# Kernel tuning notes

Hardware: AMD Instinct MI355X
Metric: run time of the kernel (lower is better)

## Reference

```python
import jax, jax.numpy as jnp
import numpy as np

B, T, D = 4, 2048, 2048
H = 16
HO = D // H  # head_out = 128


def setup_inputs() -> dict:
    key = jax.random.key(0)
    ks = jax.random.split(key, 6)
    x = jax.random.normal(ks[0], (B, T, D), dtype=jnp.float32)
    scale = 0.02
    Wq = jax.random.normal(ks[1], (D, D), dtype=jnp.float32) * scale
    Wk = jax.random.normal(ks[2], (D, D), dtype=jnp.float32) * scale
    Wv = jax.random.normal(ks[3], (D, D), dtype=jnp.float32) * scale
    Wp = jax.random.normal(ks[4], (D, D), dtype=jnp.float32) * scale
    bp = jnp.zeros((D,), dtype=jnp.float32)
    return {"x": x, "Wq": Wq, "Wk": Wk, "Wv": Wv, "Wp": Wp, "bp": bp}


def reference(x, Wq, Wk, Wv, Wp, bp):
    b, t, _ = x.shape
    # QKV projections (weights stored [d_in, d_out])
    q = x @ Wq
    k = x @ Wk
    v = x @ Wv
    split = lambda a: a.reshape(b, t, H, HO).transpose(0, 2, 1, 3)  # [b,H,T,ho]
    qh, kh, vh = split(q), split(k), split(v)
    # Feature attention: contract over tokens -> [b,H,ho,ho]
    scores = jnp.einsum('bhtf,bhtg->bhfg', qh, kh) / jnp.sqrt(jnp.float32(HO))
    weights = jax.nn.softmax(scores, axis=-1)  # dropout p=0.0 (identity)
    # feature_alibi: [1/T, 1/(T-1), ..., 1], broadcast over batch/head/feature
    feat_alibi = (1.0 / jnp.arange(t, 0, -1, dtype=jnp.float32)).reshape(1, 1, t, 1)
    vh = vh + feat_alibi
    # (weights @ v^T)^T : ctx[b,h,t,f] = sum_g weights[b,h,f,g] * v[b,h,t,g]
    ctx = jnp.einsum('bhfg,bhtg->bhtf', weights, vh)
    ctx = ctx.transpose(0, 2, 1, 3).reshape(b, t, H * HO)  # [b,T,d_out]
    return ctx @ Wp + bp
```

## Files before the change

kernel.cpp:

```cpp
#include <hip/hip_runtime.h>
#include <hip/hip_bf16.h>


#define Tt 2048
#define Dd 2048
#define Mm 8192

typedef __attribute__((ext_vector_type(4))) float f32x4;
typedef __attribute__((ext_vector_type(8))) short s16x8;
static_assert(sizeof(s16x8) == 16, "frag size");

typedef const __attribute__((address_space(1))) void* gptr_t;
typedef __attribute__((address_space(3))) void* lptr_t;

__device__ __forceinline__ float bf2f(ushort u) {
    union { unsigned int i; float f; } c; c.i = ((unsigned int)u) << 16; return c.f;
}
__device__ __forceinline__ ushort f2bf(float f) {
    union { float f; unsigned int i; } c; c.f = f;
    return (ushort)((c.i + 0x7FFFu + ((c.i >> 16) & 1u)) >> 16);
}
__device__ __forceinline__ void gload16(const void* g, void* l) {
    __builtin_amdgcn_global_load_lds((gptr_t)g, (lptr_t)l, 16, 0, 0);
}
__device__ __forceinline__ s16x8 ldfrag(const char* p) { return *(const s16x8*)p; }

#define MFMA_BF16(d, a, b) \
    d = __builtin_amdgcn_mfma_f32_16x16x32_bf16((a), (b), (d), 0, 0, 0)


__global__ __launch_bounds__(256) void convxT_kernel(const float* __restrict__ x,
        ushort* __restrict__ xb, ushort* __restrict__ xT) {
    __shared__ float tile[64][65];
    const int b = blockIdx.z;
    const int t0 = blockIdx.y * 64, d0 = blockIdx.x * 64;
    const int r4 = threadIdx.x >> 6, c = threadIdx.x & 63;
#pragma unroll
    for (int i = 0; i < 16; i++) {
        const int row = i * 4 + r4;
        const size_t g = ((size_t)b * Tt + t0 + row) * Dd + d0 + c;
        const float val = x[g];
        xb[g] = f2bf(val);
        tile[row][c] = val;
    }
    __syncthreads();
#pragma unroll
    for (int i = 0; i < 16; i++) {
        const int row = i * 4 + r4;
        xT[(size_t)b * ((size_t)Dd * Tt) + (size_t)(d0 + row) * Tt + t0 + c] =
            f2bf(tile[c][row]);
    }
}


__global__ __launch_bounds__(256) void transw_kernel(const float* __restrict__ W0,
        const float* __restrict__ W1, const float* __restrict__ W2,
        const float* __restrict__ W3, ushort* __restrict__ Wt,
        float* __restrict__ S) {
    __shared__ float tile[64][65];
    const int z = blockIdx.z;
    const float* W = (z == 0) ? W0 : (z == 1) ? W1 : (z == 2) ? W2 : W3;
    ushort* dst = Wt + (size_t)z * ((size_t)Dd * Dd);
    const int n0 = blockIdx.x * 64, k0 = blockIdx.y * 64;
    const int r4 = threadIdx.x >> 6, c = threadIdx.x & 63;
#pragma unroll
    for (int i = 0; i < 16; i++) {
        const int row = i * 4 + r4;
        tile[row][c] = W[(size_t)(k0 + row) * Dd + n0 + c];
    }
    __syncthreads();
#pragma unroll
    for (int i = 0; i < 16; i++) {
        const int row = i * 4 + r4;
        dst[(size_t)(n0 + row) * Dd + k0 + c] = f2bf(tile[c][row]);
    }
    if (z == 3) {
        float partial = 0.f;
#pragma unroll
        for (int i = 0; i < 16; i++) partial += tile[r4 * 16 + i][c];
        atomicAdd(&S[n0 + c], partial);
    }
}


__device__ __forceinline__ void stage_half(char* ldsRegion, const ushort* gRegion,
                                           int ld, int half, int tid) {
#pragma unroll
    for (int j = 0; j < 2; j++) {
        const int Pb = half * 16384 + j * 8192 + (tid >> 6) * 1024;
        const int P = Pb + (tid & 63) * 16;
        const int row = P >> 7;
        const int colb = (P ^ ((row & 7) << 4)) & 127;
        gload16(gRegion + (size_t)row * ld + (colb >> 1), ldsRegion + Pb);
    }
}

template <int MODE>
__global__ __launch_bounds__(512, 2) void gemm256_kernel(
        const ushort* __restrict__ A, const ushort* __restrict__ Bt,
        void* __restrict__ Cv, const float* __restrict__ bias,
        const float* __restrict__ S,
        int Kdim, int lda, int ldb, int ldc,
        size_t astride, size_t bstride, size_t cstride) {
    extern __shared__ char lds[];

    const int tid = threadIdx.x;
    const int lane = tid & 63;
    const int w = tid >> 6;
    const int wr = w >> 2, wc = w & 3;
    const int fr = lane & 15, fq = lane >> 4;

    const int bid = blockIdx.x;
    const int cpx = (int)gridDim.x >> 3;
    const int wg = (bid & 7) * cpx + (bid >> 3);
    const int m0 = (wg >> 3) * 256;
    const int n0 = (wg & 7) * 256;

    const ushort* Ag = A + (size_t)blockIdx.z * astride + (size_t)m0 * lda;
    const ushort* Bg = Bt + (size_t)blockIdx.z * bstride + (size_t)n0 * ldb;
    const int NT = Kdim >> 6;

    const int aoff = wr * 16384 + fr * 128;
    const int boff = wc * 8192 + fr * 128;
    const int xo = (fr & 7) << 4;
    const int cp0 = (fq * 16) ^ xo;
    const int cp1 = (64 + fq * 16) ^ xo;

    char* buf0 = lds;
    char* buf1 = lds + 65536;
    const char* Ab0 = buf0 + aoff;
    const char* Bb0 = buf0 + 32768 + boff;
    const char* Ab1 = buf1 + aoff;
    const char* Bb1 = buf1 + 32768 + boff;

    f32x4 acc[8][4];
#pragma unroll
    for (int i = 0; i < 8; i++)
#pragma unroll
        for (int j = 0; j < 4; j++) acc[i][j] = {0.f, 0.f, 0.f, 0.f};

    s16x8 afX[4][2], afY[4][2], bf01[2][2], bf23[2][2];

    {
        stage_half(buf0,         Ag, lda, 0, tid);
        stage_half(buf0,         Ag, lda, 1, tid);
        stage_half(buf0 + 32768, Bg, ldb, 0, tid);
        stage_half(buf0 + 32768, Bg, ldb, 1, tid);
        stage_half(buf1,         Ag + 64, lda, 0, tid);
        stage_half(buf1,         Ag + 64, lda, 1, tid);
        stage_half(buf1 + 32768, Bg + 64, ldb, 0, tid);
        stage_half(buf1 + 32768, Bg + 64, ldb, 1, tid);
        __builtin_amdgcn_sched_barrier(0);
        asm volatile("s_waitcnt vmcnt(8)" ::: "memory");
        __builtin_amdgcn_s_barrier();
    }

    const int NI = NT >> 1;
    for (int j = 0; j < NI; ++j) {
        const int e = 2 * j;
        const bool sAo = (j > 0);
        const bool sE2 = (e + 2 < NT);
        const bool sO2 = (e + 3 < NT);
        const ushort* AgO  = Ag + (size_t)(e + 1) * 64;
        const ushort* AgE2 = Ag + (size_t)(e + 2) * 64;
        const ushort* BgE2 = Bg + (size_t)(e + 2) * 64;
        const ushort* BgO2 = Bg + (size_t)(e + 3) * 64;

#pragma unroll
        for (int m = 0; m < 4; m++) {
            afX[m][0] = ldfrag(Ab0 + m * 2048 + cp0);
            afX[m][1] = ldfrag(Ab0 + m * 2048 + cp1);
        }
#pragma unroll
        for (int n = 0; n < 2; n++) {
            bf01[n][0] = ldfrag(Bb0 + n * 2048 + cp0);
            bf01[n][1] = ldfrag(Bb0 + n * 2048 + cp1);
        }
        if (sAo) stage_half(buf1, AgO, lda, 0, tid);
        __builtin_amdgcn_sched_barrier(0);
        asm volatile("s_waitcnt lgkmcnt(8)" ::: "memory");
        __builtin_amdgcn_s_barrier();
        asm volatile("s_waitcnt lgkmcnt(0)" ::: "memory");
        __builtin_amdgcn_sched_barrier(0);
        __builtin_amdgcn_s_setprio(1);
#pragma unroll
        for (int k = 0; k < 2; k++)
#pragma unroll
            for (int m = 0; m < 4; m++)
#pragma unroll
                for (int n = 0; n < 2; n++) MFMA_BF16(acc[m][n], afX[m][k], bf01[n][k]);
        __builtin_amdgcn_s_setprio(0);
        __builtin_amdgcn_s_barrier();

#pragma unroll
        for (int n = 0; n < 2; n++) {
            bf23[n][0] = ldfrag(Bb0 + (n + 2) * 2048 + cp0);
            bf23[n][1] = ldfrag(Bb0 + (n + 2) * 2048 + cp1);
        }
        if (sAo) stage_half(buf1, AgO, lda, 1, tid);
        __builtin_amdgcn_sched_barrier(0);
        __builtin_amdgcn_s_barrier();
        asm volatile("s_waitcnt lgkmcnt(0)" ::: "memory");
        __builtin_amdgcn_sched_barrier(0);
        __builtin_amdgcn_s_setprio(1);
#pragma unroll
        for (int k = 0; k < 2; k++)
#pragma unroll
            for (int m = 0; m < 4; m++)
#pragma unroll
                for (int n = 0; n < 2; n++) MFMA_BF16(acc[m][n + 2], afX[m][k], bf23[n][k]);
        __builtin_amdgcn_s_setprio(0);
        __builtin_amdgcn_s_barrier();

#pragma unroll
        for (int m = 0; m < 4; m++) {
            afY[m][0] = ldfrag(Ab0 + (m + 4) * 2048 + cp0);
            afY[m][1] = ldfrag(Ab0 + (m + 4) * 2048 + cp1);
        }
        if (sE2) stage_half(buf0 + 32768, BgE2, ldb, 0, tid);
        __builtin_amdgcn_sched_barrier(0);
        __builtin_amdgcn_s_barrier();
        asm volatile("s_waitcnt lgkmcnt(0)" ::: "memory");
        __builtin_amdgcn_sched_barrier(0);
        __builtin_amdgcn_s_setprio(1);
#pragma unroll
        for (int k = 0; k < 2; k++)
#pragma unroll
            for (int m = 0; m < 4; m++)
#pragma unroll
                for (int n = 0; n < 2; n++) MFMA_BF16(acc[m + 4][n], afY[m][k], bf01[n][k]);
        __builtin_amdgcn_s_setprio(0);
        __builtin_amdgcn_s_barrier();

        if (sE2) stage_half(buf0 + 32768, BgE2, ldb, 1, tid);
        __builtin_amdgcn_sched_barrier(0);
        __builtin_amdgcn_s_setprio(1);
#pragma unroll
        for (int k = 0; k < 2; k++)
#pragma unroll
            for (int m = 0; m < 4; m++)
#pragma unroll
                for (int n = 0; n < 2; n++) MFMA_BF16(acc[m + 4][n + 2], afY[m][k], bf23[n][k]);
        __builtin_amdgcn_s_setprio(0);
        __builtin_amdgcn_sched_barrier(0);
        if (sE2) asm volatile("s_waitcnt vmcnt(4)" ::: "memory");
        else     asm volatile("s_waitcnt vmcnt(0)" ::: "memory");
        __builtin_amdgcn_s_barrier();

#pragma unroll
        for (int m = 0; m < 4; m++) {
            afX[m][0] = ldfrag(Ab1 + m * 2048 + cp0);
            afX[m][1] = ldfrag(Ab1 + m * 2048 + cp1);
        }
#pragma unroll
        for (int n = 0; n < 2; n++) {
            bf01[n][0] = ldfrag(Bb1 + n * 2048 + cp0);
            bf01[n][1] = ldfrag(Bb1 + n * 2048 + cp1);
        }
        if (sE2) stage_half(buf0, AgE2, lda, 0, tid);
        __builtin_amdgcn_sched_barrier(0);
        asm volatile("s_waitcnt lgkmcnt(8)" ::: "memory");
        __builtin_amdgcn_s_barrier();
        asm volatile("s_waitcnt lgkmcnt(0)" ::: "memory");
        __builtin_amdgcn_sched_barrier(0);
        __builtin_amdgcn_s_setprio(1);
#pragma unroll
        for (int k = 0; k < 2; k++)
#pragma unroll
            for (int m = 0; m < 4; m++)
#pragma unroll
                for (int n = 0; n < 2; n++) MFMA_BF16(acc[m][n], afX[m][k], bf01[n][k]);
        __builtin_amdgcn_s_setprio(0);
        __builtin_amdgcn_s_barrier();

#pragma unroll
        for (int n = 0; n < 2; n++) {
            bf23[n][0] = ldfrag(Bb1 + (n + 2) * 2048 + cp0);
            bf23[n][1] = ldfrag(Bb1 + (n + 2) * 2048 + cp1);
        }
        if (sE2) stage_half(buf0, AgE2, lda, 1, tid);
        __builtin_amdgcn_sched_barrier(0);
        __builtin_amdgcn_s_barrier();
        asm volatile("s_waitcnt lgkmcnt(0)" ::: "memory");
        __builtin_amdgcn_sched_barrier(0);
        __builtin_amdgcn_s_setprio(1);
#pragma unroll
        for (int k = 0; k < 2; k++)
#pragma unroll
            for (int m = 0; m < 4; m++)
#pragma unroll
                for (int n = 0; n < 2; n++) MFMA_BF16(acc[m][n + 2], afX[m][k], bf23[n][k]);
        __builtin_amdgcn_s_setprio(0);
        __builtin_amdgcn_s_barrier();

#pragma unroll
        for (int m = 0; m < 4; m++) {
            afY[m][0] = ldfrag(Ab1 + (m + 4) * 2048 + cp0);
            afY[m][1] = ldfrag(Ab1 + (m + 4) * 2048 + cp1);
        }
        if (sO2) stage_half(buf1 + 32768, BgO2, ldb, 0, tid);
        __builtin_amdgcn_sched_barrier(0);
        __builtin_amdgcn_s_barrier();
        asm volatile("s_waitcnt lgkmcnt(0)" ::: "memory");
        __builtin_amdgcn_sched_barrier(0);
        __builtin_amdgcn_s_setprio(1);
#pragma unroll
        for (int k = 0; k < 2; k++)
#pragma unroll
            for (int m = 0; m < 4; m++)
#pragma unroll
                for (int n = 0; n < 2; n++) MFMA_BF16(acc[m + 4][n], afY[m][k], bf01[n][k]);
        __builtin_amdgcn_s_setprio(0);
        __builtin_amdgcn_s_barrier();

        if (sO2) stage_half(buf1 + 32768, BgO2, ldb, 1, tid);
        __builtin_amdgcn_sched_barrier(0);
        __builtin_amdgcn_s_setprio(1);
#pragma unroll
        for (int k = 0; k < 2; k++)
#pragma unroll
            for (int m = 0; m < 4; m++)
#pragma unroll
                for (int n = 0; n < 2; n++) MFMA_BF16(acc[m + 4][n + 2], afY[m][k], bf23[n][k]);
        __builtin_amdgcn_s_setprio(0);
        __builtin_amdgcn_sched_barrier(0);
        if (sO2) asm volatile("s_waitcnt vmcnt(4)" ::: "memory");
        else     asm volatile("s_waitcnt vmcnt(0)" ::: "memory");
        __builtin_amdgcn_s_barrier();
    }

    if (MODE == 2) {
        float* C = (float*)Cv + (size_t)blockIdx.z * cstride;
#pragma unroll
        for (int mi = 0; mi < 8; mi++)
#pragma unroll
            for (int ni = 0; ni < 4; ni++)
#pragma unroll
                for (int r = 0; r < 4; r++) {
                    const int row = m0 + wr * 128 + mi * 16 + fq * 4 + r;
                    const int col = n0 + wc * 64 + ni * 16 + fr;
                    const float alibi = 1.0f / (float)(Tt - row);
                    C[(size_t)row * ldc + col] =
                        acc[mi][ni][r] + alibi * S[col] + bias[col];
                }
    } else {
        ushort* C = (ushort*)Cv + (size_t)blockIdx.z * cstride;
#pragma unroll
        for (int mi = 0; mi < 8; mi++)
#pragma unroll
            for (int ni = 0; ni < 4; ni++)
#pragma unroll
                for (int r = 0; r < 4; r++) {
                    const int row = m0 + wr * 128 + mi * 16 + fq * 4 + r;
                    const int col = n0 + wc * 64 + ni * 16 + fr;
                    C[(size_t)row * ldc + col] = f2bf(acc[mi][ni][r]);
                }
    }
}


template <int MODE>
__global__ __launch_bounds__(256, 2) void gemm_kernel(
        const ushort* __restrict__ A, const ushort* __restrict__ Bt,
        void* __restrict__ Cv,
        int Kdim, int lda, int ldb, int ldc) {
    __shared__ ushort lsA[128 * 32];
    __shared__ ushort lsB[128 * 32];

    const int tid = threadIdx.x;
    const int w = tid >> 6, lane = tid & 63;
    const int m0 = blockIdx.y * 128;
    const int n0 = blockIdx.x * 128;

    const ushort* Ab = A;
    const ushort* Bb = Bt;
    size_t coff = 0;
    if (MODE == 3) {
        const int z = blockIdx.z, s = z >> 6, bh = z & 63;
        const int b = bh >> 4, h = bh & 15;
        Ab += (size_t)h * 128 * Dd + (size_t)s * 512;
        Bb += (size_t)b * ((size_t)Dd * Dd) + (size_t)h * 128 * Dd + (size_t)s * 512;
        coff = (size_t)s * (64 * 16384) + (size_t)bh * 16384;
    }
    if (MODE == 4) {
        const int z = blockIdx.z, b = z >> 4, h = z & 15;
        Ab += (size_t)h * 128;
        Bb += (size_t)z * 16384;
        coff = (size_t)b * ((size_t)Dd * Dd) + (size_t)h * 128;
    }

    const int sr = lane >> 2;
    const int sc = (lane & 3) * 8;
    const int c0 = w, c1 = w + 4;
    const int rA0 = c0 * 16 + sr, rA1 = c1 * 16 + sr;

    const int fr = lane & 15, fq = lane >> 4;
    const int wr = (w >> 1) * 64, wc = (w & 1) * 64;

    f32x4 acc[4][4];
#pragma unroll
    for (int i = 0; i < 4; i++)
#pragma unroll
        for (int j = 0; j < 4; j++) acc[i][j] = {0.f, 0.f, 0.f, 0.f};

    for (int kt = 0; kt < Kdim; kt += 32) {
        gload16(Ab + (size_t)(m0 + rA0) * lda + kt + sc, lsA + c0 * 512);
        gload16(Ab + (size_t)(m0 + rA1) * lda + kt + sc, lsA + c1 * 512);
        gload16(Bb + (size_t)(n0 + rA0) * ldb + kt + sc, lsB + c0 * 512);
        gload16(Bb + (size_t)(n0 + rA1) * ldb + kt + sc, lsB + c1 * 512);
        __syncthreads();

        s16x8 afrag[4], bfrag[4];
#pragma unroll
        for (int i = 0; i < 4; i++)
            afrag[i] = *(const s16x8*)(lsA + (wr + i * 16 + fr) * 32 + fq * 8);
#pragma unroll
        for (int j = 0; j < 4; j++)
            bfrag[j] = *(const s16x8*)(lsB + (wc + j * 16 + fr) * 32 + fq * 8);
#pragma unroll
        for (int i = 0; i < 4; i++)
#pragma unroll
            for (int j = 0; j < 4; j++)
                MFMA_BF16(acc[i][j], afrag[i], bfrag[j]);
        __syncthreads();
    }

    if (MODE == 3) {
        float* C = (float*)Cv + coff;
#pragma unroll
        for (int i = 0; i < 4; i++)
#pragma unroll
            for (int j = 0; j < 4; j++)
#pragma unroll
                for (int r = 0; r < 4; r++) {
                    const int row = m0 + wr + i * 16 + fq * 4 + r;
                    const int col = n0 + wc + j * 16 + fr;
                    C[(size_t)row * ldc + col] = acc[i][j][r];
                }
    } else {
        ushort* C = (ushort*)Cv + coff;
#pragma unroll
        for (int i = 0; i < 4; i++)
#pragma unroll
            for (int j = 0; j < 4; j++)
#pragma unroll
                for (int r = 0; r < 4; r++) {
                    const int row = m0 + wr + i * 16 + fq * 4 + r;
                    const int col = n0 + wc + j * 16 + fr;
                    C[(size_t)row * ldc + col] = f2bf(acc[i][j][r]);
                }
    }
}


__global__ __launch_bounds__(256) void softmax_kernel(const float* __restrict__ part,
                                                      ushort* __restrict__ wtsT) {
    const int tid = threadIdx.x;
    const int wv = tid >> 6, lane = tid & 63;
    const int row = blockIdx.x * 4 + wv;
    const float* p = part + (size_t)row * 128 + lane * 2;
    float v0 = 0.f, v1 = 0.f;
#pragma unroll
    for (int s = 0; s < 4; s++) {
        const float2 t = *(const float2*)(p + (size_t)s * 1048576);
        v0 += t.x; v1 += t.y;
    }
    const float sc = 0.088388347648318447f;
    v0 *= sc; v1 *= sc;
    float m = fmaxf(v0, v1);
#pragma unroll
    for (int off = 32; off > 0; off >>= 1) m = fmaxf(m, __shfl_xor(m, off));
    const float e0 = __expf(v0 - m), e1 = __expf(v1 - m);
    float smv = e0 + e1;
#pragma unroll
    for (int off = 32; off > 0; off >>= 1) smv += __shfl_xor(smv, off);
    const float inv = 1.0f / smv;
    const int bh = row >> 7, f = row & 127;
    ushort* o = wtsT + (size_t)bh * 16384 + (size_t)(lane * 2) * 128 + f;
    o[0]   = f2bf(e0 * inv);
    o[128] = f2bf(e1 * inv);
}


extern "C" void kernel_launch(void* const* d_in, const int* in_sizes, int n_in,
                              void* d_out, int out_size, void* d_ws, size_t ws_size,
                              hipStream_t stream) {
    const float* x  = (const float*)d_in[0];
    const float* Wq = (const float*)d_in[1];
    const float* Wk = (const float*)d_in[2];
    const float* Wv = (const float*)d_in[3];
    const float* Wp = (const float*)d_in[4];
    const float* bp = (const float*)d_in[5];
    float* out = (float*)d_out;
    char* ws = (char*)d_ws;

    ushort* xb   = (ushort*)(ws);
    ushort* xT   = (ushort*)(ws + (32ull << 20));
    ushort* Wt   = (ushort*)(ws + (64ull << 20));
    ushort* G    = (ushort*)(ws + (96ull << 20));
    ushort* Hb   = (ushort*)(ws + (128ull << 20));
    ushort* v    = (ushort*)(ws + (160ull << 20));
    float*  part = (float*) (ws + (96ull << 20));
    ushort* wtsT = (ushort*)(ws + (112ull << 20));
    float*  S    = (float*) (ws + (194ull << 20));
    ushort* Mt   = xT;

    const size_t WSZ = (size_t)Dd * Dd;
    const size_t TD  = (size_t)Tt * Dd;

    static_cast<void>(hipFuncSetAttribute((const void*)gemm256_kernel<0>,
        hipFuncAttributeMaxDynamicSharedMemorySize, 131072));
    static_cast<void>(hipFuncSetAttribute((const void*)gemm256_kernel<2>,
        hipFuncAttributeMaxDynamicSharedMemorySize, 131072));

    static_cast<void>(hipMemsetAsync(S, 0, Dd * sizeof(float), stream));
    convxT_kernel<<<dim3(32, 32, 4), 256, 0, stream>>>(x, xb, xT);
    transw_kernel<<<dim3(32, 32, 4), 256, 0, stream>>>(Wq, Wk, Wv, Wp, Wt, S);

    gemm256_kernel<0><<<dim3(64, 1, 4), 512, 131072, stream>>>(
        xT, xT, G, nullptr, nullptr, 2048, 2048, 2048, 2048, WSZ, WSZ, WSZ);

    gemm256_kernel<0><<<dim3(64, 1, 4), 512, 131072, stream>>>(
        Wt + WSZ, G, Hb, nullptr, nullptr, 2048, 2048, 2048, 2048, 0, WSZ, WSZ);

    gemm256_kernel<0><<<dim3(256, 1, 1), 512, 131072, stream>>>(
        xb, Wt + 2 * WSZ, v, nullptr, nullptr, 2048, 2048, 2048, 2048, 0, 0, 0);

    gemm_kernel<3><<<dim3(1, 1, 256), 256, 0, stream>>>(
        Wt, Hb, part, 512, 2048, 2048, 128);

    softmax_kernel<<<2048, 256, 0, stream>>>(part, wtsT);

    gemm_kernel<4><<<dim3(1, 16, 64), 256, 0, stream>>>(
        Wt + 3 * WSZ, wtsT, Mt, 128, 2048, 128, 2048);

    gemm256_kernel<2><<<dim3(64, 1, 4), 512, 131072, stream>>>(
        v, Mt, out, bp, S, 2048, 2048, 2048, 2048, TD, WSZ, TD);
}
```

Measured before the change: 353.2 us.

## Replace 256x256 GEMM with simpler 128x128 double-buffered tile kernel

Swaps the 512-thread 256x256-tile GEMM, with its finely interleaved half-tile staging schedule, for a 256-thread 128x128-tile kernel. The new kernel does one full-tile fragment load and one MFMA phase per K step over a plain two-buffer pipeline, and uses half the LDS. Grids grow fourfold, giving more workgroups per GPU and possibly higher occupancy. In exchange, each tile gets less operand reuse, and the overlap between LDS reads, global prefetch and MFMA work is coarser.

After: 373.4 us. +5.7%, slower.

```diff
diff --git a/kernel.cpp b/kernel.cpp
--- a/kernel.cpp
+++ b/kernel.cpp
@@ -83,20 +83,19 @@
 }
 
 
-__device__ __forceinline__ void stage_half(char* ldsRegion, const ushort* gRegion,
-                                           int ld, int half, int tid) {
-#pragma unroll
-    for (int j = 0; j < 2; j++) {
-        const int Pb = half * 16384 + j * 8192 + (tid >> 6) * 1024;
+__device__ __forceinline__ void stage_tile(char* region, const ushort* g, int ld, int tid) {
+#pragma unroll
+    for (int j = 0; j < 4; j++) {
+        const int Pb = j * 4096 + (tid >> 6) * 1024;
         const int P = Pb + (tid & 63) * 16;
         const int row = P >> 7;
         const int colb = (P ^ ((row & 7) << 4)) & 127;
-        gload16(gRegion + (size_t)row * ld + (colb >> 1), ldsRegion + Pb);
+        gload16(g + (size_t)row * ld + (colb >> 1), region + Pb);
     }
 }
 
 template <int MODE>
-__global__ __launch_bounds__(512, 2) void gemm256_kernel(
+__global__ __launch_bounds__(256, 2) void gemm128_kernel(
         const ushort* __restrict__ A, const ushort* __restrict__ Bt,
         void* __restrict__ Cv, const float* __restrict__ bias,
         const float* __restrict__ S,
@@ -107,79 +106,57 @@
     const int tid = threadIdx.x;
     const int lane = tid & 63;
     const int w = tid >> 6;
-    const int wr = w >> 2, wc = w & 3;
+    const int wr = w >> 1, wc = w & 1;
     const int fr = lane & 15, fq = lane >> 4;
 
     const int bid = blockIdx.x;
     const int cpx = (int)gridDim.x >> 3;
     const int wg = (bid & 7) * cpx + (bid >> 3);
-    const int m0 = (wg >> 3) * 256;
-    const int n0 = (wg & 7) * 256;
+    const int m0 = (wg >> 4) * 128;
+    const int n0 = (wg & 15) * 128;
 
     const ushort* Ag = A + (size_t)blockIdx.z * astride + (size_t)m0 * lda;
     const ushort* Bg = Bt + (size_t)blockIdx.z * bstride + (size_t)n0 * ldb;
     const int NT = Kdim >> 6;
 
-    const int aoff = wr * 16384 + fr * 128;
-    const int boff = wc * 8192 + fr * 128;
+    const int aoff = (wr * 64 + fr) * 128;
+    const int boff = (wc * 64 + fr) * 128;
     const int xo = (fr & 7) << 4;
     const int cp0 = (fq * 16) ^ xo;
     const int cp1 = (64 + fq * 16) ^ xo;
 
-    char* buf0 = lds;
-    char* buf1 = lds + 65536;
-    const char* Ab0 = buf0 + aoff;
-    const char* Bb0 = buf0 + 32768 + boff;
-    const char* Ab1 = buf1 + aoff;
-    const char* Bb1 = buf1 + 32768 + boff;
-
-    f32x4 acc[8][4];
-#pragma unroll
-    for (int i = 0; i < 8; i++)
+    f32x4 acc[4][4];
+#pragma unroll
+    for (int i = 0; i < 4; i++)
 #pragma unroll
         for (int j = 0; j < 4; j++) acc[i][j] = {0.f, 0.f, 0.f, 0.f};
 
-    s16x8 afX[4][2], afY[4][2], bf01[2][2], bf23[2][2];
-
-    {
-        stage_half(buf0,         Ag, lda, 0, tid);
-        stage_half(buf0,         Ag, lda, 1, tid);
-        stage_half(buf0 + 32768, Bg, ldb, 0, tid);
-        stage_half(buf0 + 32768, Bg, ldb, 1, tid);
-        stage_half(buf1,         Ag + 64, lda, 0, tid);
-        stage_half(buf1,         Ag + 64, lda, 1, tid);
-        stage_half(buf1 + 32768, Bg + 64, ldb, 0, tid);
-        stage_half(buf1 + 32768, Bg + 64, ldb, 1, tid);
+    s16x8 af[4][2], bf[4][2];
+
+    stage_tile(lds,         Ag,      lda, tid);
+    stage_tile(lds + 16384, Bg,      ldb, tid);
+    stage_tile(lds + 32768, Ag + 64, lda, tid);
+    stage_tile(lds + 49152, Bg + 64, ldb, tid);
+    __builtin_amdgcn_sched_barrier(0);
+    asm volatile("s_waitcnt vmcnt(8)" ::: "memory");
+    __builtin_amdgcn_s_barrier();
+
+    for (int t = 0; t < NT; ++t) {
+        char* buf = lds + (t & 1) * 32768;
+        const char* Ab = buf + aoff;
+        const char* Bb = buf + 16384 + boff;
+
+#pragma unroll
+        for (int m = 0; m < 4; m++) {
+            af[m][0] = ldfrag(Ab + m * 2048 + cp0);
+            af[m][1] = ldfrag(Ab + m * 2048 + cp1);
+        }
+#pragma unroll
+        for (int n = 0; n < 4; n++) {
+            bf[n][0] = ldfrag(Bb + n * 2048 + cp0);
+            bf[n][1] = ldfrag(Bb + n * 2048 + cp1);
+        }
         __builtin_amdgcn_sched_barrier(0);
-        asm volatile("s_waitcnt vmcnt(8)" ::: "memory");
-        __builtin_amdgcn_s_barrier();
-    }
-
-    const int NI = NT >> 1;
-    for (int j = 0; j < NI; ++j) {
-        const int e = 2 * j;
-        const bool sAo = (j > 0);
-        const bool sE2 = (e + 2 < NT);
-        const bool sO2 = (e + 3 < NT);
-        const ushort* AgO  = Ag + (size_t)(e + 1) * 64;
-        const ushort* AgE2 = Ag + (size_t)(e + 2) * 64;
-        const ushort* BgE2 = Bg + (size_t)(e + 2) * 64;
-        const ushort* BgO2 = Bg + (size_t)(e + 3) * 64;
-
-#pragma unroll
-        for (int m = 0; m < 4; m++) {
-            afX[m][0] = ldfrag(Ab0 + m * 2048 + cp0);
-            afX[m][1] = ldfrag(Ab0 + m * 2048 + cp1);
-        }
-#pragma unroll
-        for (int n = 0; n < 2; n++) {
-            bf01[n][0] = ldfrag(Bb0 + n * 2048 + cp0);
-            bf01[n][1] = ldfrag(Bb0 + n * 2048 + cp1);
-        }
-        if (sAo) stage_half(buf1, AgO, lda, 0, tid);
-        __builtin_amdgcn_sched_barrier(0);
-        asm volatile("s_waitcnt lgkmcnt(8)" ::: "memory");
-        __builtin_amdgcn_s_barrier();
         asm volatile("s_waitcnt lgkmcnt(0)" ::: "memory");
         __builtin_amdgcn_sched_barrier(0);
         __builtin_amdgcn_s_setprio(1);
@@ -188,156 +165,29 @@
 #pragma unroll
             for (int m = 0; m < 4; m++)
 #pragma unroll
-                for (int n = 0; n < 2; n++) MFMA_BF16(acc[m][n], afX[m][k], bf01[n][k]);
+                for (int n = 0; n < 4; n++) MFMA_BF16(acc[m][n], af[m][k], bf[n][k]);
         __builtin_amdgcn_s_setprio(0);
         __builtin_amdgcn_s_barrier();
 
-#pragma unroll
-        for (int n = 0; n < 2; n++) {
-            bf23[n][0] = ldfrag(Bb0 + (n + 2) * 2048 + cp0);
-            bf23[n][1] = ldfrag(Bb0 + (n + 2) * 2048 + cp1);
+        if (t + 2 < NT) {
+            stage_tile(buf,         Ag + (size_t)(t + 2) * 64, lda, tid);
+            stage_tile(buf + 16384, Bg + (size_t)(t + 2) * 64, ldb, tid);
         }
-        if (sAo) stage_half(buf1, AgO, lda, 1, tid);
         __builtin_amdgcn_sched_barrier(0);
-        __builtin_amdgcn_s_barrier();
-        asm volatile("s_waitcnt lgkmcnt(0)" ::: "memory");
-        __builtin_amdgcn_sched_barrier(0);
-        __builtin_amdgcn_s_setprio(1);
-#pragma unroll
-        for (int k = 0; k < 2; k++)
-#pragma unroll
-            for (int m = 0; m < 4; m++)
-#pragma unroll
-                for (int n = 0; n < 2; n++) MFMA_BF16(acc[m][n + 2], afX[m][k], bf23[n][k]);
-        __builtin_amdgcn_s_setprio(0);
-        __builtin_amdgcn_s_barrier();
-
-#pragma unroll
-        for (int m = 0; m < 4; m++) {
-            afY[m][0] = ldfrag(Ab0 + (m + 4) * 2048 + cp0);
-            afY[m][1] = ldfrag(Ab0 + (m + 4) * 2048 + cp1);
-        }
-        if (sE2) stage_half(buf0 + 32768, BgE2, ldb, 0, tid);
-        __builtin_amdgcn_sched_barrier(0);
-        __builtin_amdgcn_s_barrier();
-        asm volatile("s_waitcnt lgkmcnt(0)" ::: "memory");
-        __builtin_amdgcn_sched_barrier(0);
-        __builtin_amdgcn_s_setprio(1);
-#pragma unroll
-        for (int k = 0; k < 2; k++)
-#pragma unroll
-            for (int m = 0; m < 4; m++)
-#pragma unroll
-                for (int n = 0; n < 2; n++) MFMA_BF16(acc[m + 4][n], afY[m][k], bf01[n][k]);
-        __builtin_amdgcn_s_setprio(0);
-        __builtin_amdgcn_s_barrier();
-
-        if (sE2) stage_half(buf0 + 32768, BgE2, ldb, 1, tid);
-        __builtin_amdgcn_sched_barrier(0);
-        __builtin_amdgcn_s_setprio(1);
-#pragma unroll
-        for (int k = 0; k < 2; k++)
-#pragma unroll
-            for (int m = 0; m < 4; m++)
-#pragma unroll
-                for (int n = 0; n < 2; n++) MFMA_BF16(acc[m + 4][n + 2], afY[m][k], bf23[n][k]);
-        __builtin_amdgcn_s_setprio(0);
-        __builtin_amdgcn_sched_barrier(0);
-        if (sE2) asm volatile("s_waitcnt vmcnt(4)" ::: "memory");
-        else     asm volatile("s_waitcnt vmcnt(0)" ::: "memory");
-        __builtin_amdgcn_s_barrier();
-
-#pragma unroll
-        for (int m = 0; m < 4; m++) {
-            afX[m][0] = ldfrag(Ab1 + m * 2048 + cp0);
-            afX[m][1] = ldfrag(Ab1 + m * 2048 + cp1);
-        }
-#pragma unroll
-        for (int n = 0; n < 2; n++) {
-            bf01[n][0] = ldfrag(Bb1 + n * 2048 + cp0);
-            bf01[n][1] = ldfrag(Bb1 + n * 2048 + cp1);
-        }
-        if (sE2) stage_half(buf0, AgE2, lda, 0, tid);
-        __builtin_amdgcn_sched_barrier(0);
-        asm volatile("s_waitcnt lgkmcnt(8)" ::: "memory");
-        __builtin_amdgcn_s_barrier();
-        asm volatile("s_waitcnt lgkmcnt(0)" ::: "memory");
-        __builtin_amdgcn_sched_barrier(0);
-        __builtin_amdgcn_s_setprio(1);
-#pragma unroll
-        for (int k = 0; k < 2; k++)
-#pragma unroll
-            for (int m = 0; m < 4; m++)
-#pragma unroll
-                for (int n = 0; n < 2; n++) MFMA_BF16(acc[m][n], afX[m][k], bf01[n][k]);
-        __builtin_amdgcn_s_setprio(0);
-        __builtin_amdgcn_s_barrier();
-
-#pragma unroll
-        for (int n = 0; n < 2; n++) {
-            bf23[n][0] = ldfrag(Bb1 + (n + 2) * 2048 + cp0);
-            bf23[n][1] = ldfrag(Bb1 + (n + 2) * 2048 + cp1);
-        }
-        if (sE2) stage_half(buf0, AgE2, lda, 1, tid);
-        __builtin_amdgcn_sched_barrier(0);
-        __builtin_amdgcn_s_barrier();
-        asm volatile("s_waitcnt lgkmcnt(0)" ::: "memory");
-        __builtin_amdgcn_sched_barrier(0);
-        __builtin_amdgcn_s_setprio(1);
-#pragma unroll
-        for (int k = 0; k < 2; k++)
-#pragma unroll
-            for (int m = 0; m < 4; m++)
-#pragma unroll
-                for (int n = 0; n < 2; n++) MFMA_BF16(acc[m][n + 2], afX[m][k], bf23[n][k]);
-        __builtin_amdgcn_s_setprio(0);
-        __builtin_amdgcn_s_barrier();
-
-#pragma unroll
-        for (int m = 0; m < 4; m++) {
-            afY[m][0] = ldfrag(Ab1 + (m + 4) * 2048 + cp0);
-            afY[m][1] = ldfrag(Ab1 + (m + 4) * 2048 + cp1);
-        }
-        if (sO2) stage_half(buf1 + 32768, BgO2, ldb, 0, tid);
-        __builtin_amdgcn_sched_barrier(0);
-        __builtin_amdgcn_s_barrier();
-        asm volatile("s_waitcnt lgkmcnt(0)" ::: "memory");
-        __builtin_amdgcn_sched_barrier(0);
-        __builtin_amdgcn_s_setprio(1);
-#pragma unroll
-        for (int k = 0; k < 2; k++)
-#pragma unroll
-            for (int m = 0; m < 4; m++)
-#pragma unroll
-                for (int n = 0; n < 2; n++) MFMA_BF16(acc[m + 4][n], afY[m][k], bf01[n][k]);
-        __builtin_amdgcn_s_setprio(0);
-        __builtin_amdgcn_s_barrier();
-
-        if (sO2) stage_half(buf1 + 32768, BgO2, ldb, 1, tid);
-        __builtin_amdgcn_sched_barrier(0);
-        __builtin_amdgcn_s_setprio(1);
-#pragma unroll
-        for (int k = 0; k < 2; k++)
-#pragma unroll
-            for (int m = 0; m < 4; m++)
-#pragma unroll
-                for (int n = 0; n < 2; n++) MFMA_BF16(acc[m + 4][n + 2], afY[m][k], bf23[n][k]);
-        __builtin_amdgcn_s_setprio(0);
-        __builtin_amdgcn_sched_barrier(0);
-        if (sO2) asm volatile("s_waitcnt vmcnt(4)" ::: "memory");
-        else     asm volatile("s_waitcnt vmcnt(0)" ::: "memory");
+        if (t + 2 < NT) asm volatile("s_waitcnt vmcnt(8)" ::: "memory");
+        else            asm volatile("s_waitcnt vmcnt(0)" ::: "memory");
         __builtin_amdgcn_s_barrier();
     }
 
     if (MODE == 2) {
         float* C = (float*)Cv + (size_t)blockIdx.z * cstride;
 #pragma unroll
-        for (int mi = 0; mi < 8; mi++)
+        for (int mi = 0; mi < 4; mi++)
 #pragma unroll
             for (int ni = 0; ni < 4; ni++)
 #pragma unroll
                 for (int r = 0; r < 4; r++) {
-                    const int row = m0 + wr * 128 + mi * 16 + fq * 4 + r;
+                    const int row = m0 + wr * 64 + mi * 16 + fq * 4 + r;
                     const int col = n0 + wc * 64 + ni * 16 + fr;
                     const float alibi = 1.0f / (float)(Tt - row);
                     C[(size_t)row * ldc + col] =
@@ -346,12 +196,12 @@
     } else {
         ushort* C = (ushort*)Cv + (size_t)blockIdx.z * cstride;
 #pragma unroll
-        for (int mi = 0; mi < 8; mi++)
+        for (int mi = 0; mi < 4; mi++)
 #pragma unroll
             for (int ni = 0; ni < 4; ni++)
 #pragma unroll
                 for (int r = 0; r < 4; r++) {
-                    const int row = m0 + wr * 128 + mi * 16 + fq * 4 + r;
+                    const int row = m0 + wr * 64 + mi * 16 + fq * 4 + r;
                     const int col = n0 + wc * 64 + ni * 16 + fr;
                     C[(size_t)row * ldc + col] = f2bf(acc[mi][ni][r]);
                 }
@@ -508,22 +358,22 @@
     const size_t WSZ = (size_t)Dd * Dd;
     const size_t TD  = (size_t)Tt * Dd;
 
-    static_cast<void>(hipFuncSetAttribute((const void*)gemm256_kernel<0>,
-        hipFuncAttributeMaxDynamicSharedMemorySize, 131072));
-    static_cast<void>(hipFuncSetAttribute((const void*)gemm256_kernel<2>,
-        hipFuncAttributeMaxDynamicSharedMemorySize, 131072));
+    static_cast<void>(hipFuncSetAttribute((const void*)gemm128_kernel<0>,
+        hipFuncAttributeMaxDynamicSharedMemorySize, 65536));
+    static_cast<void>(hipFuncSetAttribute((const void*)gemm128_kernel<2>,
+        hipFuncAttributeMaxDynamicSharedMemorySize, 65536));
 
     static_cast<void>(hipMemsetAsync(S, 0, Dd * sizeof(float), stream));
     convxT_kernel<<<dim3(32, 32, 4), 256, 0, stream>>>(x, xb, xT);
     transw_kernel<<<dim3(32, 32, 4), 256, 0, stream>>>(Wq, Wk, Wv, Wp, Wt, S);
 
-    gemm256_kernel<0><<<dim3(64, 1, 4), 512, 131072, stream>>>(
+    gemm128_kernel<0><<<dim3(256, 1, 4), 256, 65536, stream>>>(
         xT, xT, G, nullptr, nullptr, 2048, 2048, 2048, 2048, WSZ, WSZ, WSZ);
 
-    gemm256_kernel<0><<<dim3(64, 1, 4), 512, 131072, stream>>>(
+    gemm128_kernel<0><<<dim3(256, 1, 4), 256, 65536, stream>>>(
         Wt + WSZ, G, Hb, nullptr, nullptr, 2048, 2048, 2048, 2048, 0, WSZ, WSZ);
 
-    gemm256_kernel<0><<<dim3(256, 1, 1), 512, 131072, stream>>>(
+    gemm128_kernel<0><<<dim3(1024, 1, 1), 256, 65536, stream>>>(
         xb, Wt + 2 * WSZ, v, nullptr, nullptr, 2048, 2048, 2048, 2048, 0, 0, 0);
 
     gemm_kernel<3><<<dim3(1, 1, 256), 256, 0, stream>>>(
@@ -534,6 +384,6 @@
     gemm_kernel<4><<<dim3(1, 16, 64), 256, 0, stream>>>(
         Wt + 3 * WSZ, wtsT, Mt, 128, 2048, 128, 2048);
 
-    gemm256_kernel<2><<<dim3(64, 1, 4), 512, 131072, stream>>>(
+    gemm128_kernel<2><<<dim3(256, 1, 4), 256, 65536, stream>>>(
         v, Mt, out, bp, S, 2048, 2048, 2048, 2048, TD, WSZ, TD);
 }
```
